# Optimization experiments

Hardware: AMD Instinct MI355X
Metric: run time of the kernel (lower is better)

Reference implementation:

```python
import jax, jax.numpy as jnp
import numpy as np

B, F, N = 64, 32, 36
REGION, HIDDEN, ATT = 1024, 1024, 1024
FEAT2 = REGION + 2 * HIDDEN  # temp_attn feat_size = 3072


def setup_inputs() -> dict:
    key = jax.random.key(0)
    ks = jax.random.split(key, 12)
    s = 0.02
    return {
        "frame_feats": jax.random.normal(ks[0], (B, F, 2 * HIDDEN), jnp.float32),
        "object_feats": jax.random.normal(ks[1], (B, F, N, REGION), jnp.float32),
        "hidden_state": jax.random.normal(ks[2], (B, HIDDEN), jnp.float32),
        # spatial attention params (torch Linear: y = x @ W.T + b)
        "s_wh_w": jax.random.normal(ks[3], (ATT, HIDDEN), jnp.float32) * s,
        "s_wh_b": jnp.zeros((ATT,), jnp.float32),
        "s_wv_w": jax.random.normal(ks[4], (ATT, REGION), jnp.float32) * s,
        "s_wv_b": jnp.zeros((ATT,), jnp.float32),
        "s_wa_w": jax.random.normal(ks[5], (ATT,), jnp.float32) * s,
        # temporal attention params (att_size = hidden_size here)
        "t_wh_w": jax.random.normal(ks[6], (HIDDEN, HIDDEN), jnp.float32) * s,
        "t_wh_b": jnp.zeros((HIDDEN,), jnp.float32),
        "t_wv_w": jax.random.normal(ks[7], (HIDDEN, FEAT2), jnp.float32) * s,
        "t_wv_b": jnp.zeros((HIDDEN,), jnp.float32),
        "t_wa_w": jax.random.normal(ks[8], (HIDDEN,), jnp.float32) * s,
    }


def reference(frame_feats, object_feats, hidden_state,
              s_wh_w, s_wh_b, s_wv_w, s_wv_b, s_wa_w,
              t_wh_w, t_wh_b, t_wv_w, t_wv_b, t_wa_w):
    # ---- spatial attention over num_boxes, per (batch, frame) ----
    # v: [B,F,N,ATT]; key proj broadcasts over frames and boxes
    v = jnp.einsum('bfnd,ad->bfna', object_feats, s_wv_w) + s_wv_b
    h = hidden_state @ s_wh_w.T + s_wh_b            # [B,ATT]
    score = jnp.tanh(v + h[:, None, None, :]) @ s_wa_w  # [B,F,N]
    alpha = jax.nn.softmax(score, axis=-1)
    obj_att = jnp.einsum('bfn,bfnd->bfd', alpha, object_feats)  # [B,F,REGION]

    # ---- temporal attention over frames ----
    feat = jnp.concatenate([obj_att, frame_feats], axis=-1)     # [B,F,FEAT2]
    v2 = jnp.einsum('bfd,ad->bfa', feat, t_wv_w) + t_wv_b       # [B,F,HIDDEN]
    h2 = hidden_state @ t_wh_w.T + t_wh_b                       # [B,HIDDEN]
    score2 = jnp.tanh(v2 + h2[:, None, :]) @ t_wa_w             # [B,F]
    beta = jax.nn.softmax(score2, axis=-1)
    loc_feat = jnp.einsum('bf,bfd->bd', beta, feat)             # [B,FEAT2]
    return loc_feat
```

## Files before the change

kernel.cpp:

```cpp
#include <hip/hip_runtime.h>
#include <hip/hip_bf16.h>
#include <stdint.h>

#define BATCH  64
#define NFRAME 32
#define NBOX   36
#define REGION 1024
#define HIDDEN 1024
#define ATTSZ  1024
#define FEAT2  3072
#define M_S (BATCH * NFRAME * NBOX)
#define M_T (BATCH * NFRAME)

typedef __attribute__((ext_vector_type(8))) short bf16x8;
typedef __attribute__((ext_vector_type(4))) float f32x4;

__device__ __forceinline__ unsigned short f2bf(float f) {
  union { float f; uint32_t u; } v; v.f = f;
  return (unsigned short)((v.u + 0x7FFFu + ((v.u >> 16) & 1u)) >> 16);
}
__device__ __forceinline__ float bf2f(unsigned short u) {
  union { uint32_t u; float f; } v; v.u = (uint32_t)u << 16; return v.f;
}
__device__ __forceinline__ float fast_tanh(float x) {
  float e = __expf(2.f * x);
  return 1.f - 2.f / (e + 1.f);
}
__device__ __forceinline__ void gload_lds16(const unsigned short* g, unsigned short* l) {
  __builtin_amdgcn_global_load_lds(
      (const __attribute__((address_space(1))) unsigned int*)g,
      (__attribute__((address_space(3))) unsigned int*)l, 16, 0, 0);
}
constexpr int clog2(int v) { return v <= 1 ? 0 : 1 + clog2(v >> 1); }

__global__ __launch_bounds__(256) void cast_f32_bf16(
    const float* __restrict__ in, unsigned short* __restrict__ out, long n) {
  long i = ((long)blockIdx.x * 256 + threadIdx.x) * 8;
  if (i >= n) return;
  float4 a = *(const float4*)(in + i);
  float4 b = *(const float4*)(in + i + 4);
  ushort4 lo; lo.x = f2bf(a.x); lo.y = f2bf(a.y); lo.z = f2bf(a.z); lo.w = f2bf(a.w);
  ushort4 hi; hi.x = f2bf(b.x); hi.y = f2bf(b.y); hi.z = f2bf(b.z); hi.w = f2bf(b.w);
  *(ushort4*)(out + i) = lo;
  *(ushort4*)(out + i + 4) = hi;
}

template<int TM, int TN, bool LINGRID, int NCOLT>
__global__ __launch_bounds__(256, 3) void gemm_tanh_score(
    const unsigned short* __restrict__ A, const unsigned short* __restrict__ W,
    const float* __restrict__ hvec, const float* __restrict__ wa,
    float* __restrict__ score, int K, int rows_per_b)
{
  constexpr int BM = 2 * TM * 16;
  constexpr int BN = 2 * TN * 16;
  __shared__ __align__(16) unsigned short ldsA[BM * 64];
  __shared__ __align__(16) unsigned short ldsW[BN * 64];
  __shared__ float h_tile[BN];
  __shared__ float score_sh[2][BM];

  const int tid  = threadIdx.x;
  const int lane = tid & 63;
  const int wid  = tid >> 6;
  const int wr   = (wid >> 1) * (TM * 16);
  const int wc   = (wid & 1) * (TN * 16);
  const int l15  = lane & 15;
  const int q    = lane >> 4;
  const int rl   = l15 & 7;
  const int srow = lane >> 3;
  const int sgr  = (lane & 7) ^ srow;

  long r0; int c0;
  if (LINGRID) {
    int bid = blockIdx.x;
    int rt = (bid & 7) + (bid >> (3 + clog2(NCOLT))) * 8;
    int ct = (bid >> 3) & (NCOLT - 1);
    r0 = (long)rt * BM; c0 = ct * BN;
  } else {
    r0 = (long)blockIdx.y * BM; c0 = blockIdx.x * BN;
  }
  const int b0 = (int)(r0 / rows_per_b);

  for (int i = tid; i < BN; i += 256)
    h_tile[i] = hvec[(long)b0 * ATTSZ + c0 + i];
  float wac[TN];
  #pragma unroll
  for (int j = 0; j < TN; ++j) wac[j] = wa[c0 + wc + j * 16 + l15];

  f32x4 acc[TM][TN] = {};

  for (int k0 = 0; k0 < K; k0 += 64) {
    __syncthreads();
    #pragma unroll
    for (int it = 0; it < BM / 32; ++it) {
      int c = wid * (BM / 32) + it;
      gload_lds16(A + (r0 + c * 8 + srow) * (long)K + k0 + (sgr << 3), ldsA + c * 512);
    }
    #pragma unroll
    for (int it = 0; it < BN / 32; ++it) {
      int c = wid * (BN / 32) + it;
      gload_lds16(W + ((long)(c0 + c * 8 + srow)) * K + k0 + (sgr << 3), ldsW + c * 512);
    }
    __syncthreads();
    #pragma unroll
    for (int s = 0; s < 2; ++s) {
      bf16x8 af[TM], wf[TN];
      const int gsw = ((s * 4 + q) ^ rl) << 3;
      #pragma unroll
      for (int i = 0; i < TM; ++i)
        af[i] = *(const bf16x8*)(ldsA + (wr + i * 16 + l15) * 64 + gsw);
      #pragma unroll
      for (int j = 0; j < TN; ++j)
        wf[j] = *(const bf16x8*)(ldsW + (wc + j * 16 + l15) * 64 + gsw);
      #pragma unroll
      for (int i = 0; i < TM; ++i)
        #pragma unroll
        for (int j = 0; j < TN; ++j)
          acc[i][j] = __builtin_amdgcn_mfma_f32_16x16x32_bf16(af[i], wf[j], acc[i][j], 0, 0, 0);
    }
  }

  #pragma unroll
  for (int i = 0; i < TM; ++i) {
    #pragma unroll
    for (int r = 0; r < 4; ++r) {
      float part = 0.f;
      #pragma unroll
      for (int j = 0; j < TN; ++j) {
        float x = acc[i][j][r] + h_tile[wc + j * 16 + l15];
        part += fast_tanh(x) * wac[j];
      }
      part += __shfl_xor(part, 1); part += __shfl_xor(part, 2);
      part += __shfl_xor(part, 4); part += __shfl_xor(part, 8);
      if (l15 == 0) score_sh[wid & 1][wr + i * 16 + q * 4 + r] = part;
    }
  }
  __syncthreads();
  if (tid < BM)
    atomicAdd(score + r0 + tid, score_sh[0][tid] + score_sh[1][tid]);
}

__global__ __launch_bounds__(256) void hidden_proj(
    const float* __restrict__ hidden,
    const float* __restrict__ s_wh_w, const float* __restrict__ s_wh_b,
    const float* __restrict__ s_wv_b,
    const float* __restrict__ t_wh_w, const float* __restrict__ t_wh_b,
    const float* __restrict__ t_wv_b,
    float* __restrict__ h_s, float* __restrict__ h_t)
{
  const float *W, *b1, *b2;
  float* out;
  if (blockIdx.y == 0) { W = s_wh_w; b1 = s_wh_b; b2 = s_wv_b; out = h_s; }
  else                 { W = t_wh_w; b1 = t_wh_b; b2 = t_wv_b; out = h_t; }
  const int lane = threadIdx.x & 63;
  const int wid  = threadIdx.x >> 6;
  const int a    = blockIdx.x * 4 + wid;
  __shared__ float hs[64 * 256];
  float acc[64];
  #pragma unroll
  for (int b = 0; b < 64; ++b) acc[b] = 0.f;

  for (int dc = 0; dc < 4; ++dc) {
    __syncthreads();
    for (int i = threadIdx.x; i < 4096; i += 256) {
      int b = i >> 6, d4 = i & 63;
      *(float4*)(hs + b * 256 + d4 * 4) =
          *(const float4*)(hidden + b * 1024 + dc * 256 + d4 * 4);
    }
    __syncthreads();
    float4 w4 = *(const float4*)(W + (long)a * 1024 + dc * 256 + lane * 4);
    #pragma unroll
    for (int b = 0; b < 64; ++b) {
      float4 h4 = *(const float4*)(hs + b * 256 + lane * 4);
      acc[b] += w4.x * h4.x + w4.y * h4.y + w4.z * h4.z + w4.w * h4.w;
    }
  }
  #pragma unroll
  for (int b = 0; b < 64; ++b) {
    #pragma unroll
    for (int off = 1; off < 64; off <<= 1)
      acc[b] += __shfl_xor(acc[b], off);
  }
  float res = 0.f;
  #pragma unroll
  for (int b = 0; b < 64; ++b)
    if (lane == b) res = acc[b];
  out[lane * 1024 + a] = res + b1[a] + b2[a];
}

__global__ __launch_bounds__(256) void spatial_softmax_obj_bf16(
    const unsigned short* __restrict__ objb, const float* __restrict__ score,
    const float* __restrict__ frame, float* __restrict__ feat,
    unsigned short* __restrict__ featb)
{
  const int bf = blockIdx.x;
  __shared__ float alpha[NBOX];
  if (threadIdx.x < 64) {
    int n = threadIdx.x;
    float v = (n < NBOX) ? score[bf * NBOX + n] : -1e30f;
    float m = v;
    #pragma unroll
    for (int off = 32; off; off >>= 1) m = fmaxf(m, __shfl_xor(m, off));
    float e = (n < NBOX) ? __expf(v - m) : 0.f;
    float ssum = e;
    #pragma unroll
    for (int off = 32; off; off >>= 1) ssum += __shfl_xor(ssum, off);
    if (n < NBOX) alpha[n] = e / ssum;
  }
  __syncthreads();
  const unsigned short* base = objb + (long)bf * NBOX * REGION;
  float4 av = {0.f, 0.f, 0.f, 0.f};
  #pragma unroll 4
  for (int n = 0; n < NBOX; ++n) {
    float al = alpha[n];
    ushort4 o = *(const ushort4*)(base + n * REGION + threadIdx.x * 4);
    av.x += al * bf2f(o.x); av.y += al * bf2f(o.y);
    av.z += al * bf2f(o.z); av.w += al * bf2f(o.w);
  }
  float* frow = feat + (long)bf * FEAT2;
  unsigned short* fbrow = featb + (long)bf * FEAT2;
  *(float4*)(frow + threadIdx.x * 4) = av;
  ushort4 avb; avb.x = f2bf(av.x); avb.y = f2bf(av.y); avb.z = f2bf(av.z); avb.w = f2bf(av.w);
  *(ushort4*)(fbrow + threadIdx.x * 4) = avb;
  const float* fsrc = frame + (long)bf * 2 * HIDDEN;
  #pragma unroll
  for (int c = 0; c < 2; ++c) {
    float4 v = *(const float4*)(fsrc + (threadIdx.x + c * 256) * 4);
    *(float4*)(frow + REGION + (threadIdx.x + c * 256) * 4) = v;
    ushort4 vb; vb.x = f2bf(v.x); vb.y = f2bf(v.y); vb.z = f2bf(v.z); vb.w = f2bf(v.w);
    *(ushort4*)(fbrow + REGION + (threadIdx.x + c * 256) * 4) = vb;
  }
}

__global__ __launch_bounds__(256) void temporal_out(
    const float* __restrict__ score2, const float* __restrict__ feat,
    float* __restrict__ out)
{
  const int b = blockIdx.x;
  __shared__ float beta[NFRAME];
  if (threadIdx.x < 64) {
    int f = threadIdx.x;
    float v = (f < NFRAME) ? score2[b * NFRAME + f] : -1e30f;
    float m = v;
    #pragma unroll
    for (int off = 32; off; off >>= 1) m = fmaxf(m, __shfl_xor(m, off));
    float e = (f < NFRAME) ? __expf(v - m) : 0.f;
    float ssum = e;
    #pragma unroll
    for (int off = 32; off; off >>= 1) ssum += __shfl_xor(ssum, off);
    if (f < NFRAME) beta[f] = e / ssum;
  }
  __syncthreads();
  int col = blockIdx.y * 1024 + threadIdx.x * 4;
  float4 av = {0.f, 0.f, 0.f, 0.f};
  #pragma unroll 4
  for (int f = 0; f < NFRAME; ++f) {
    float bw = beta[f];
    float4 v = *(const float4*)(feat + (long)(b * NFRAME + f) * FEAT2 + col);
    av.x += bw * v.x; av.y += bw * v.y; av.z += bw * v.z; av.w += bw * v.w;
  }
  *(float4*)(out + (long)b * FEAT2 + col) = av;
}

#define FBM 128
#define FBN 128
#define FBK 64
#define LDKP 72
__global__ __launch_bounds__(256) void fused_gemm_tanh_score_f32(
    const float* __restrict__ A, const float* __restrict__ W,
    const float* __restrict__ hvec, const float* __restrict__ wa,
    float* __restrict__ score, int M, int K, int rows_per_b)
{
  __shared__ unsigned short ldsA[FBM * LDKP];
  __shared__ unsigned short ldsW[FBN * LDKP];
  const int tid  = threadIdx.x;
  const int lane = tid & 63;
  const int wid  = tid >> 6;
  const int wr   = (wid >> 1) * 64;
  const int wc   = (wid & 1) * 64;
  const int l15  = lane & 15;
  const int q    = lane >> 4;
  const long r0  = (long)blockIdx.y * FBM;
  const int  c0  = blockIdx.x * FBN;

  f32x4 acc[4][4] = {};
  for (int k0 = 0; k0 < K; k0 += FBK) {
    __syncthreads();
    #pragma unroll
    for (int it = 0; it < 8; ++it) {
      int c = tid + it * 256;
      int row = c >> 4, qb = c & 15;
      float4 s = *(const float4*)(A + (r0 + row) * (long)K + k0 + qb * 4);
      ushort4 d; d.x = f2bf(s.x); d.y = f2bf(s.y); d.z = f2bf(s.z); d.w = f2bf(s.w);
      *(ushort4*)(ldsA + row * LDKP + qb * 4) = d;
    }
    #pragma unroll
    for (int it = 0; it < 8; ++it) {
      int c = tid + it * 256;
      int row = c >> 4, qb = c & 15;
      float4 s = *(const float4*)(W + (c0 + row) * (long)K + k0 + qb * 4);
      ushort4 d; d.x = f2bf(s.x); d.y = f2bf(s.y); d.z = f2bf(s.z); d.w = f2bf(s.w);
      *(ushort4*)(ldsW + row * LDKP + qb * 4) = d;
    }
    __syncthreads();
    #pragma unroll
    for (int s = 0; s < 2; ++s) {
      bf16x8 af[4], bfr[4];
      #pragma unroll
      for (int i = 0; i < 4; ++i)
        af[i] = *(const bf16x8*)(ldsA + (wr + i * 16 + l15) * LDKP + s * 32 + q * 8);
      #pragma unroll
      for (int j = 0; j < 4; ++j)
        bfr[j] = *(const bf16x8*)(ldsW + (wc + j * 16 + l15) * LDKP + s * 32 + q * 8);
      #pragma unroll
      for (int i = 0; i < 4; ++i)
        #pragma unroll
        for (int j = 0; j < 4; ++j)
          acc[i][j] = __builtin_amdgcn_mfma_f32_16x16x32_bf16(af[i], bfr[j], acc[i][j], 0, 0, 0);
    }
  }
  float wac[4];
  #pragma unroll
  for (int j = 0; j < 4; ++j) wac[j] = wa[c0 + wc + j * 16 + l15];
  #pragma unroll
  for (int i = 0; i < 4; ++i) {
    #pragma unroll
    for (int r = 0; r < 4; ++r) {
      int row = (int)r0 + wr + i * 16 + q * 4 + r;
      const float* hrow = hvec + (long)(row / rows_per_b) * ATTSZ;
      float part = 0.f;
      #pragma unroll
      for (int j = 0; j < 4; ++j) {
        float x = acc[i][j][r] + hrow[c0 + wc + j * 16 + l15];
        part += fast_tanh(x) * wac[j];
      }
      part += __shfl_xor(part, 1); part += __shfl_xor(part, 2);
      part += __shfl_xor(part, 4); part += __shfl_xor(part, 8);
      if (l15 == 0) atomicAdd(score + row, part);
    }
  }
}

__global__ __launch_bounds__(256) void spatial_softmax_obj_f32(
    const float* __restrict__ obj, const float* __restrict__ score,
    const float* __restrict__ frame, float* __restrict__ feat)
{
  const int bf = blockIdx.x;
  __shared__ float alpha[NBOX];
  if (threadIdx.x < 64) {
    int n = threadIdx.x;
    float v = (n < NBOX) ? score[bf * NBOX + n] : -1e30f;
    float m = v;
    #pragma unroll
    for (int off = 32; off; off >>= 1) m = fmaxf(m, __shfl_xor(m, off));
    float e = (n < NBOX) ? __expf(v - m) : 0.f;
    float ssum = e;
    #pragma unroll
    for (int off = 32; off; off >>= 1) ssum += __shfl_xor(ssum, off);
    if (n < NBOX) alpha[n] = e / ssum;
  }
  __syncthreads();
  const float* base = obj + (long)bf * NBOX * REGION;
  float4 av = {0.f, 0.f, 0.f, 0.f};
  for (int n = 0; n < NBOX; ++n) {
    float al = alpha[n];
    float4 o = *(const float4*)(base + n * REGION + threadIdx.x * 4);
    av.x += al * o.x; av.y += al * o.y; av.z += al * o.z; av.w += al * o.w;
  }
  float* frow = feat + (long)bf * FEAT2;
  *(float4*)(frow + threadIdx.x * 4) = av;
  const float4* fsrc = (const float4*)(frame + (long)bf * 2 * HIDDEN);
  float4* fdst = (float4*)(frow + REGION);
  fdst[threadIdx.x]       = fsrc[threadIdx.x];
  fdst[threadIdx.x + 256] = fsrc[threadIdx.x + 256];
}

__global__ __launch_bounds__(256) void temporal_out_f32(
    const float* __restrict__ score2, const float* __restrict__ feat,
    float* __restrict__ out)
{
  const int b = blockIdx.x;
  __shared__ float beta[NFRAME];
  if (threadIdx.x < 64) {
    int f = threadIdx.x;
    float v = (f < NFRAME) ? score2[b * NFRAME + f] : -1e30f;
    float m = v;
    #pragma unroll
    for (int off = 32; off; off >>= 1) m = fmaxf(m, __shfl_xor(m, off));
    float e = (f < NFRAME) ? __expf(v - m) : 0.f;
    float ssum = e;
    #pragma unroll
    for (int off = 32; off; off >>= 1) ssum += __shfl_xor(ssum, off);
    if (f < NFRAME) beta[f] = e / ssum;
  }
  __syncthreads();
  #pragma unroll
  for (int c = 0; c < 3; ++c) {
    int col = (threadIdx.x + c * 256) * 4;
    float4 av = {0.f, 0.f, 0.f, 0.f};
    for (int f = 0; f < NFRAME; ++f) {
      float bw = beta[f];
      float4 v = *(const float4*)(feat + (long)(b * NFRAME + f) * FEAT2 + col);
      av.x += bw * v.x; av.y += bw * v.y; av.z += bw * v.z; av.w += bw * v.w;
    }
    *(float4*)(out + (long)b * FEAT2 + col) = av;
  }
}

extern "C" void kernel_launch(void* const* d_in, const int* in_sizes, int n_in,
                              void* d_out, int out_size, void* d_ws, size_t ws_size,
                              hipStream_t stream) {
  const float* frame  = (const float*)d_in[0];
  const float* obj    = (const float*)d_in[1];
  const float* hidden = (const float*)d_in[2];
  const float* s_wh_w = (const float*)d_in[3];
  const float* s_wh_b = (const float*)d_in[4];
  const float* s_wv_w = (const float*)d_in[5];
  const float* s_wv_b = (const float*)d_in[6];
  const float* s_wa_w = (const float*)d_in[7];
  const float* t_wh_w = (const float*)d_in[8];
  const float* t_wh_b = (const float*)d_in[9];
  const float* t_wv_w = (const float*)d_in[10];
  const float* t_wv_b = (const float*)d_in[11];
  const float* t_wa_w = (const float*)d_in[12];
  float* out = (float*)d_out;

  char* p = (char*)d_ws;
  auto alloc = [&](size_t bytes) { char* r = p; p += (bytes + 255) & ~255ull; return r; };
  float* h_s     = (float*)alloc(65536 * 4);
  float* h_t     = (float*)alloc(65536 * 4);
  float* score_s = (float*)alloc((size_t)M_S * 4);
  float* score2  = (float*)alloc((size_t)M_T * 4);
  float* feat    = (float*)alloc((size_t)M_T * FEAT2 * 4);
  unsigned short* objb  = (unsigned short*)alloc((size_t)M_S * REGION * 2);
  unsigned short* featb = (unsigned short*)alloc((size_t)M_T * FEAT2 * 2);
  unsigned short* wvsb  = (unsigned short*)alloc((size_t)ATTSZ * REGION * 2);
  unsigned short* wvtb  = (unsigned short*)alloc((size_t)HIDDEN * FEAT2 * 2);
  size_t needed = (size_t)(p - (char*)d_ws);
  bool fast = needed <= ws_size;

  hipMemsetAsync(score_s, 0, (size_t)(M_S + M_T) * sizeof(float), stream);
  hidden_proj<<<dim3(256, 2), 256, 0, stream>>>(
      hidden, s_wh_w, s_wh_b, s_wv_b, t_wh_w, t_wh_b, t_wv_b, h_s, h_t);

  if (fast) {
    cast_f32_bf16<<<(M_S * (long)REGION) / 2048, 256, 0, stream>>>(obj, objb, (long)M_S * REGION);
    cast_f32_bf16<<<(ATTSZ * (long)REGION) / 2048, 256, 0, stream>>>(s_wv_w, wvsb, (long)ATTSZ * REGION);
    cast_f32_bf16<<<(HIDDEN * (long)FEAT2) / 2048, 256, 0, stream>>>(t_wv_w, wvtb, (long)HIDDEN * FEAT2);

    gemm_tanh_score<4, 4, true, 8><<<dim3(8 * (M_S / 128)), 256, 0, stream>>>(
        objb, wvsb, h_s, s_wa_w, score_s, REGION, NFRAME * NBOX);

    spatial_softmax_obj_bf16<<<M_T, 256, 0, stream>>>(objb, score_s, frame, feat, featb);

    gemm_tanh_score<1, 4, false, 8><<<dim3(8, M_T / 32), 256, 0, stream>>>(
        featb, wvtb, h_t, t_wa_w, score2, FEAT2, NFRAME);

    temporal_out<<<dim3(BATCH, 3), 256, 0, stream>>>(score2, feat, out);
  } else {
    fused_gemm_tanh_score_f32<<<dim3(8, M_S / FBM), 256, 0, stream>>>(
        obj, s_wv_w, h_s, s_wa_w, score_s, M_S, REGION, NFRAME * NBOX);
    spatial_softmax_obj_f32<<<M_T, 256, 0, stream>>>(obj, score_s, frame, feat);
    fused_gemm_tanh_score_f32<<<dim3(8, M_T / FBM), 256, 0, stream>>>(
        feat, t_wv_w, h_t, t_wa_w, score2, M_T, FEAT2, NFRAME);
    temporal_out_f32<<<BATCH, 256, 0, stream>>>(score2, feat, out);
  }
}
```

Measured before the change: 736.2 us.

## Add 8-wave 256x256 pipelined bf16 GEMM for spatial attention scoring

Replaces the spatial-attention GEMM+tanh+score kernel with a new 512-thread kernel that uses 256x256 tiles and double-buffered LDS stages split into K-halves. Direct global-to-LDS loads are interleaved with MFMA phases, and the LDS layout is swizzled. It also raises wave priority around the MFMA bursts and remaps block indices for L2 reuse. The goal is higher MFMA utilization and more data reuse per block in the dominant GEMM, at the cost of more register and LDS pressure and hand-tuned vmcnt waits that are fragile if the load counts ever change.

After: 786.7 us. +6.9%, slower.

```diff
diff --git a/kernel.cpp b/kernel.cpp
--- a/kernel.cpp
+++ b/kernel.cpp
@@ -43,6 +43,143 @@
   ushort4 hi; hi.x = f2bf(b.x); hi.y = f2bf(b.y); hi.z = f2bf(b.z); hi.w = f2bf(b.w);
   *(ushort4*)(out + i) = lo;
   *(ushort4*)(out + i + 4) = hi;
+}
+
+__global__ __launch_bounds__(512, 2) void gemm8_tanh_score(
+    const unsigned short* __restrict__ A, const unsigned short* __restrict__ W,
+    const float* __restrict__ hvec, const float* __restrict__ wa,
+    float* __restrict__ score)
+{
+  constexpr int BM = 256;
+  constexpr int BN = 256;
+  __shared__ __align__(16) unsigned short lds[2][2][2][BM * 32];
+  __shared__ float h_tile[2][BN];
+  __shared__ float score_sh[4][BM];
+
+  const int tid  = threadIdx.x;
+  const int lane = tid & 63;
+  const int wid  = tid >> 6;
+  const int wm   = wid >> 2;
+  const int wn   = wid & 3;
+  const int wr   = wm * 128;
+  const int wc   = wn * 64;
+  const int l15  = lane & 15;
+  const int q    = lane >> 4;
+  const int skey = (l15 >> 1) & 3;
+  const int srow = lane >> 2;
+  const int sg   = (lane & 3) ^ ((lane >> 3) & 3);
+
+  const int bid = blockIdx.x;
+  const int rt  = (bid & 7) + (bid >> 5) * 8;
+  const int ct  = (bid >> 3) & 3;
+  const long r0 = (long)rt * BM;
+  const int  c0 = ct * BN;
+  const int  b0 = (int)(r0 / (NFRAME * NBOX));
+  const int  b1 = (b0 + 1 <= BATCH - 1) ? b0 + 1 : BATCH - 1;
+  const int  bnd = (b0 + 1) * (NFRAME * NBOX) - (int)r0;
+
+  {
+    int s = tid >> 8, i = tid & 255;
+    int bb = s ? b1 : b0;
+    h_tile[s][i] = hvec[(long)bb * ATTSZ + c0 + i];
+  }
+  float wac[4];
+  #pragma unroll
+  for (int j = 0; j < 4; ++j) wac[j] = wa[c0 + wc + j * 16 + l15];
+
+  f32x4 acc[8][4] = {};
+
+  auto stage = [&](int buf, int op, int kh, int tile) {
+    const unsigned short* src = op ? W : A;
+    const long base = op ? (long)c0 : r0;
+    #pragma unroll
+    for (int cc = 0; cc < 2; ++cc) {
+      int chunk = wid * 2 + cc;
+      gload_lds16(src + (base + chunk * 16 + srow) * 1024 + tile * 64 + kh * 32 + sg * 8,
+                  &lds[buf][op][kh][chunk * 512]);
+    }
+  };
+
+#define PH(BUF, KS, MH, LOADB, SB, SOP, SKH, STILE, LAST) do {               \
+    bf16x8 af_[4];                                                            \
+    if (LOADB) {                                                              \
+      _Pragma("unroll")                                                       \
+      for (int j = 0; j < 4; ++j)                                             \
+        bf_[j] = *(const bf16x8*)&lds[BUF][1][KS]                             \
+            [(wc + j * 16 + l15) * 32 + ((q ^ skey) * 8)];                    \
+    }                                                                         \
+    _Pragma("unroll")                                                         \
+    for (int i = 0; i < 4; ++i)                                               \
+      af_[i] = *(const bf16x8*)&lds[BUF][0][KS]                               \
+          [(wr + (MH) * 64 + i * 16 + l15) * 32 + ((q ^ skey) * 8)];          \
+    stage(SB, SOP, SKH, STILE);                                               \
+    __builtin_amdgcn_s_barrier();                                             \
+    __builtin_amdgcn_s_setprio(1);                                            \
+    _Pragma("unroll")                                                         \
+    for (int i = 0; i < 4; ++i) {                                             \
+      _Pragma("unroll")                                                       \
+      for (int j = 0; j < 4; ++j)                                             \
+        acc[(MH) * 4 + i][j] = __builtin_amdgcn_mfma_f32_16x16x32_bf16(       \
+            af_[i], bf_[j], acc[(MH) * 4 + i][j], 0, 0, 0);                   \
+    }                                                                         \
+    __builtin_amdgcn_s_setprio(0);                                            \
+    if (LAST) asm volatile("s_waitcnt vmcnt(4)" ::: "memory");                \
+    __builtin_amdgcn_s_barrier();                                             \
+  } while (0)
+
+  stage(0, 0, 0, 0); stage(0, 1, 0, 0); stage(0, 0, 1, 0); stage(0, 1, 1, 0);
+  stage(1, 0, 0, 1); stage(1, 1, 0, 1);
+  asm volatile("s_waitcnt vmcnt(4)" ::: "memory");
+  __builtin_amdgcn_s_barrier();
+
+  #pragma unroll 1
+  for (int tt = 0; tt < 8; ++tt) {
+    const int ta = (2 * tt + 1) & 15;
+    const int tb = (2 * tt + 2) & 15;
+    const int tc = (2 * tt + 3) & 15;
+    {
+      bf16x8 bf_[4];
+      PH(0, 0, 0, true,  1, 0, 1, ta, false);
+      PH(0, 0, 1, false, 1, 1, 1, ta, false);
+      PH(0, 1, 0, true,  0, 0, 0, tb, false);
+      PH(0, 1, 1, false, 0, 1, 0, tb, true);
+    }
+    {
+      bf16x8 bf_[4];
+      PH(1, 0, 0, true,  0, 0, 1, tb, false);
+      PH(1, 0, 1, false, 0, 1, 1, tb, false);
+      PH(1, 1, 0, true,  1, 0, 0, tc, false);
+      PH(1, 1, 1, false, 1, 1, 0, tc, true);
+    }
+  }
+#undef PH
+
+  __syncthreads();
+
+  #pragma unroll
+  for (int mh = 0; mh < 2; ++mh) {
+    #pragma unroll
+    for (int i = 0; i < 4; ++i) {
+      #pragma unroll
+      for (int r = 0; r < 4; ++r) {
+        int rowt = wr + mh * 64 + i * 16 + q * 4 + r;
+        const float* hrow = h_tile[rowt >= bnd ? 1 : 0];
+        float part = 0.f;
+        #pragma unroll
+        for (int j = 0; j < 4; ++j) {
+          float x = acc[mh * 4 + i][j][r] + hrow[wc + j * 16 + l15];
+          part += fast_tanh(x) * wac[j];
+        }
+        part += __shfl_xor(part, 1); part += __shfl_xor(part, 2);
+        part += __shfl_xor(part, 4); part += __shfl_xor(part, 8);
+        if (l15 == 0) score_sh[wn][rowt] = part;
+      }
+    }
+  }
+  __syncthreads();
+  if (tid < BM)
+    atomicAdd(score + r0 + tid,
+              score_sh[0][tid] + score_sh[1][tid] + score_sh[2][tid] + score_sh[3][tid]);
 }
 
 template<int TM, int TN, bool LINGRID, int NCOLT>
@@ -447,8 +584,8 @@
     cast_f32_bf16<<<(ATTSZ * (long)REGION) / 2048, 256, 0, stream>>>(s_wv_w, wvsb, (long)ATTSZ * REGION);
     cast_f32_bf16<<<(HIDDEN * (long)FEAT2) / 2048, 256, 0, stream>>>(t_wv_w, wvtb, (long)HIDDEN * FEAT2);
 
-    gemm_tanh_score<4, 4, true, 8><<<dim3(8 * (M_S / 128)), 256, 0, stream>>>(
-        objb, wvsb, h_s, s_wa_w, score_s, REGION, NFRAME * NBOX);
+    gemm8_tanh_score<<<dim3(8 * (M_S / 256) / 2), 512, 0, stream>>>(
+        objb, wvsb, h_s, s_wa_w, score_s);
 
     spatial_softmax_obj_bf16<<<M_T, 256, 0, stream>>>(objb, score_s, frame, feat, featb);
 
```
